# Kernel optimization log

Measured on AMD Instinct MI355X. Metric: run time of the kernel, lower is better.

## Reference

```python
import jax, jax.numpy as jnp
import numpy as np

N, C_IN, C_OUT, NS, SP = 100000, 64, 64, 16, 8
MID = C_OUT
EPS = 1e-5


def _bn(t, g, b):
    # BatchNorm1d training-mode stats over (n, k) per channel (biased var, as torch)
    m = t.mean(axis=(0, 1))
    v = t.var(axis=(0, 1))
    return g * (t - m) / jnp.sqrt(v + EPS) + b


def setup_inputs() -> dict:
    key = jax.random.key(0)
    ks = jax.random.split(key, 24)
    s = 0.05
    d = {
        'p': jax.random.normal(ks[0], (N, 3), jnp.float32),
        'x': jax.random.normal(ks[1], (N, C_IN), jnp.float32),
        'knn_idx': jax.random.randint(ks[2], (N, NS), 0, N, jnp.int64),
        # channelMixMLPs01: Linear(3+in, ns) + Bilinear(ns, ns, ns)
        'w1': jax.random.normal(ks[3], (NS, 3 + C_IN), jnp.float32) * s,
        'b1': jnp.zeros((NS,), jnp.float32),
        'bw': jax.random.normal(ks[4], (NS, NS, NS), jnp.float32) * s,
        'bb': jnp.zeros((NS,), jnp.float32),
        # linear_p: Linear(3,3) -> BN(3) -> ReLU -> Linear(3,out)
        'lp_w1': jax.random.normal(ks[5], (3, 3), jnp.float32) * s,
        'lp_b1': jnp.zeros((3,), jnp.float32),
        'bnp_g': jnp.ones((3,), jnp.float32),
        'bnp_b': jnp.zeros((3,), jnp.float32),
        'lp_w2': jax.random.normal(ks[6], (C_OUT, 3), jnp.float32) * s,
        'lp_b2': jnp.zeros((C_OUT,), jnp.float32),
        'c1_w': jax.random.normal(ks[7], (MID, 2 * NS), jnp.float32) * s,
        'bn1_g': jnp.ones((MID,), jnp.float32),
        'bn1_b': jnp.zeros((MID,), jnp.float32),
        'c2_w': jax.random.normal(ks[8], (MID // SP, MID), jnp.float32) * s,
        'bn2_g': jnp.ones((MID // SP,), jnp.float32),
        'bn2_b': jnp.zeros((MID // SP,), jnp.float32),
        'c3_w': jax.random.normal(ks[9], (C_OUT // SP, MID // SP), jnp.float32) * s,
        'c3_b': jnp.zeros((C_OUT // SP,), jnp.float32),
        # channelMixMLPs03: Linear(in, out)
        'w3': jax.random.normal(ks[10], (C_OUT, C_IN), jnp.float32) * s,
        'b3': jnp.zeros((C_OUT,), jnp.float32),
    }
    return d


def reference(p, x, knn_idx, w1, b1, bw, bb, lp_w1, lp_b1, bnp_g, bnp_b,
              lp_w2, lp_b2, c1_w, bn1_g, bn1_b, c2_w, bn2_g, bn2_b,
              c3_w, c3_b, w3, b3):
    n = p.shape[0]
    # queryandgroup (use_xyz=True): gather neighbors, relative coords + feats
    p_r = p[knn_idx] - p[:, None, :]                 # [n, k, 3]
    x_knn = jnp.concatenate([p_r, x[knn_idx]], -1)   # [n, k, 3+c_in]
    # channelMixMLPs01: Linear -> ReLU -> Bilinear(e, e)
    e = jax.nn.relu(x_knn @ w1.T + b1)               # [n, k, ns]
    e = jnp.einsum('nki,oij,nkj->nko', e, bw, e) + bb
    # linear_p on relative coords
    pe = p_r @ lp_w1.T + lp_b1                       # [n, k, 3]
    pe = jax.nn.relu(_bn(pe, bnp_g, bnp_b))
    p_embed = pe @ lp_w2.T + lp_b2                   # [n, k, out]
    # shrink_p: n k (a b) -> sum over a -> [n, k, ns]
    p_shrink = p_embed.reshape(n, NS, C_OUT // NS, NS).sum(axis=2)
    energy = jnp.concatenate([e, p_shrink], -1)
    # channelMixMLPs02 (1x1 convs == per-point linears over channel dim)
    h = jax.nn.relu(_bn(energy @ c1_w.T, bn1_g, bn1_b))
    h = jax.nn.relu(_bn(h @ c2_w.T, bn2_g, bn2_b))
    w = jax.nn.softmax(h @ c3_w.T + c3_b, axis=1)    # [n, k, out/sp]
    # value path: Linear then gather by knn_idx
    x_v = (x @ w3.T + b3)[knn_idx]                   # [n, k, out]
    xk = (x_v + p_embed).reshape(n, NS, SP, C_OUT // SP)
    xk = (xk * w[:, :, None, :]).reshape(n, NS, C_OUT)
    x_out = xk.sum(axis=1)                           # [n, out]
    return (x_out, xk, knn_idx, p_r)
```

## Files before the change

### kernel.cpp

```cpp
#include <hip/hip_runtime.h>
#include <math.h>

#define NPTS 100000
#define KNB  16
#define NK   1600000

#define OUT_XK   6400000
#define OUT_KNN  108800000
#define OUT_PR   110400000

#define WS_BNP_RAW 0
#define WS_BN2_RAW 134
#define WS_BNP_SS  160
#define WS_WS2     166
#define WS_WSB     214
#define WS_BN1_SS  230
#define WS_BN2_SS  358
#define WS_SYM     384
#define WS_C1F     2560
#define WS_C2T     2816
#define WS_GRAM    4096
#define WS_E       8192
#define WS_T2      25608192
#define WS_XROW    38408192
#define WS_X1      44808192

#define GRID_NK 3125
#define NK_STRIDE 800000

#define TA_PACK ((1ULL<<15)|(1ULL<<18)|(1ULL<<21)|(1ULL<<24)|(2ULL<<27)|(2ULL<<30)|(2ULL<<33)|(3ULL<<36)|(3ULL<<39)|(4ULL<<42))
#define TB_PACK ((1ULL<<3)|(2ULL<<6)|(3ULL<<9)|(4ULL<<12)|(1ULL<<15)|(2ULL<<18)|(3ULL<<21)|(4ULL<<24)|(2ULL<<27)|(3ULL<<30)|(4ULL<<33)|(3ULL<<36)|(4ULL<<39)|(4ULL<<42))


__global__ __launch_bounds__(256) void k_pre(
    const float* __restrict__ x, const float* __restrict__ w3,
    const float* __restrict__ b3, const float* __restrict__ w1,
    const float* __restrict__ b1, float* __restrict__ ws)
{
    int n = blockIdx.x * 256 + threadIdx.x;
    if (n >= NPTS) return;
    float xr[64];
    const float4* xp = (const float4*)(x + (size_t)n * 64);
    #pragma unroll
    for (int i = 0; i < 16; ++i) {
        float4 v = xp[i];
        xr[4*i] = v.x; xr[4*i+1] = v.y; xr[4*i+2] = v.z; xr[4*i+3] = v.w;
    }
    float* xrow = ws + WS_XROW;
    for (int c = 0; c < 64; ++c) {
        const float* wr = w3 + c * 64;
        float a0 = b3[c], a1 = 0.f;
        #pragma unroll
        for (int q = 0; q < 64; q += 2) { a0 += wr[q] * xr[q]; a1 += wr[q+1] * xr[q+1]; }
        xrow[(size_t)n * 64 + c] = a0 + a1;
    }
    float* X1 = ws + WS_X1;
    for (int j = 0; j < 16; ++j) {
        const float* wr = w1 + j * 67 + 3;
        float a0 = b1[j], a1 = 0.f;
        #pragma unroll
        for (int q = 0; q < 64; q += 2) { a0 += wr[q] * xr[q]; a1 += wr[q+1] * xr[q+1]; }
        X1[n * 16 + j] = a0 + a1;
    }
}

__global__ void k_sym(const float* __restrict__ bw, float* __restrict__ ws)
{
    int t = blockIdx.x * 256 + threadIdx.x;
    if (t >= 136 * 16) return;
    int pair = t >> 4, o = t & 15;
    int i = 0, r = pair;
    while (r >= 16 - i) { r -= 16 - i; ++i; }
    int j = i + r;
    float v = bw[o * 256 + i * 16 + j];
    if (i != j) v += bw[o * 256 + j * 16 + i];
    ws[WS_SYM + pair * 16 + o] = v;
}

__global__ __launch_bounds__(256) void k_pstats(
    const float* __restrict__ p, const int* __restrict__ knn,
    const float* __restrict__ lpw1, const float* __restrict__ lpb1,
    float* __restrict__ ws, float* __restrict__ out)
{
    float ps0=0.f, ps1=0.f, ps2=0.f, pq0=0.f, pq1=0.f, pq2=0.f;
    float* o_knn = out + OUT_KNN;
    float* o_pr  = out + OUT_PR;
    int id = blockIdx.x * 256 + threadIdx.x;
    #pragma unroll 1
    for (int it = 0; it < 2; ++it, id += NK_STRIDE) {
        int n = id >> 4;
        int idx = knn[id];
        float pr0 = p[idx*3+0] - p[n*3+0];
        float pr1 = p[idx*3+1] - p[n*3+1];
        float pr2 = p[idx*3+2] - p[n*3+2];
        o_pr[id*3+0] = pr0; o_pr[id*3+1] = pr1; o_pr[id*3+2] = pr2;
        o_knn[id] = (float)idx;
        float v0 = lpb1[0] + lpw1[0]*pr0 + lpw1[1]*pr1 + lpw1[2]*pr2;
        float v1 = lpb1[1] + lpw1[3]*pr0 + lpw1[4]*pr1 + lpw1[5]*pr2;
        float v2 = lpb1[2] + lpw1[6]*pr0 + lpw1[7]*pr1 + lpw1[8]*pr2;
        ps0 += v0; ps1 += v1; ps2 += v2;
        pq0 += v0*v0; pq1 += v1*v1; pq2 += v2*v2;
    }
    #pragma unroll
    for (int off = 32; off; off >>= 1) {
        ps0 += __shfl_xor(ps0, off); ps1 += __shfl_xor(ps1, off); ps2 += __shfl_xor(ps2, off);
        pq0 += __shfl_xor(pq0, off); pq1 += __shfl_xor(pq1, off); pq2 += __shfl_xor(pq2, off);
    }
    __shared__ float sb[6];
    if (threadIdx.x < 6) sb[threadIdx.x] = 0.f;
    __syncthreads();
    if ((threadIdx.x & 63) == 0) {
        atomicAdd(&sb[0], ps0); atomicAdd(&sb[1], ps1); atomicAdd(&sb[2], ps2);
        atomicAdd(&sb[3], pq0); atomicAdd(&sb[4], pq1); atomicAdd(&sb[5], pq2);
    }
    __syncthreads();
    if (threadIdx.x < 6) atomicAdd(&ws[WS_BNP_RAW + threadIdx.x], sb[threadIdx.x]);
}

__global__ void k_fin_bnp(float* __restrict__ ws,
    const float* __restrict__ g, const float* __restrict__ b,
    const float* __restrict__ lpw2, const float* __restrict__ lpb2)
{
    int t = threadIdx.x;
    if (t < 3) {
        float mean = ws[WS_BNP_RAW + t] / (float)NK;
        float var  = ws[WS_BNP_RAW + 3 + t] / (float)NK - mean * mean;
        float sc = g[t] * rsqrtf(var + 1e-5f);
        ws[WS_BNP_SS + t] = sc;
        ws[WS_BNP_SS + 3 + t] = b[t] - mean * sc;
    }
    if (t >= 16 && t < 64) {
        int r = t - 16, j = r / 3, d = r % 3;
        ws[WS_WS2 + r] = lpw2[(j)*3+d] + lpw2[(16+j)*3+d] + lpw2[(32+j)*3+d] + lpw2[(48+j)*3+d];
    }
    if (t >= 64 && t < 80) {
        int j = t - 64;
        ws[WS_WSB + j] = lpb2[j] + lpb2[16+j] + lpb2[32+j] + lpb2[48+j];
    }
}

__global__ void k_fold(const float* __restrict__ c1w, const float* __restrict__ c2w,
                       float* __restrict__ ws)
{
    int c = threadIdx.x;
    if (c >= 64) return;
    const float* B = c1w + c * 32 + 16;
    float m0 = 0.f, m1 = 0.f, m2 = 0.f, dd = 0.f;
    #pragma unroll
    for (int j = 0; j < 16; ++j) {
        float bj = B[j];
        m0 += bj * ws[WS_WS2 + j*3 + 0];
        m1 += bj * ws[WS_WS2 + j*3 + 1];
        m2 += bj * ws[WS_WS2 + j*3 + 2];
        dd += bj * ws[WS_WSB + j];
    }
    ws[WS_C1F + c*4 + 0] = m0;
    ws[WS_C1F + c*4 + 1] = m1;
    ws[WS_C1F + c*4 + 2] = m2;
    ws[WS_C1F + c*4 + 3] = dd;
    #pragma unroll
    for (int k = 0; k < 8; ++k)
        ws[WS_C2T + c*8 + k] = c2w[k * 64 + c];
}

__global__ __launch_bounds__(256) void k_stage0(
    const float* __restrict__ o_pr_in, const int* __restrict__ knn,
    const float* __restrict__ w1, const float* __restrict__ bb,
    const float* __restrict__ lpw1, const float* __restrict__ lpb1,
    const float* __restrict__ wsro, float* __restrict__ ws)
{
    __shared__ __align__(16) char uni[36864];
    float* e1sf  = (float*)uni;
    float* ub    = (float*)uni;
    float* gpart = (float*)(uni + 20480);
    const float* symw = wsro + WS_SYM;
    const float* X1   = wsro + WS_X1;
    float* e_out = ws + WS_E;
    int tid = threadIdx.x;

    int gid = blockIdx.x * 256 + tid;
    int id0 = gid * 2;
    float qv[2][3];

    #pragma unroll
    for (int e = 0; e < 2; ++e) {
        int id = id0 + e;
        int idx = knn[id];
        float pr0 = o_pr_in[id*3+0];
        float pr1 = o_pr_in[id*3+1];
        float pr2 = o_pr_in[id*3+2];
        float v0 = lpb1[0] + lpw1[0]*pr0 + lpw1[1]*pr1 + lpw1[2]*pr2;
        float v1 = lpb1[1] + lpw1[3]*pr0 + lpw1[4]*pr1 + lpw1[5]*pr2;
        float v2 = lpb1[2] + lpw1[6]*pr0 + lpw1[7]*pr1 + lpw1[8]*pr2;
        qv[e][0] = fmaxf(v0*wsro[WS_BNP_SS+0] + wsro[WS_BNP_SS+3], 0.f);
        qv[e][1] = fmaxf(v1*wsro[WS_BNP_SS+1] + wsro[WS_BNP_SS+4], 0.f);
        qv[e][2] = fmaxf(v2*wsro[WS_BNP_SS+2] + wsro[WS_BNP_SS+5], 0.f);
        const float4* xg = (const float4*)(X1 + (size_t)idx * 16);
        #pragma unroll
        for (int h = 0; h < 4; ++h) {
            float4 v = xg[h];
            const float* wr = w1 + (4*h) * 67;
            e1sf[e*4096 + (4*h+0)*256 + tid] = fmaxf(v.x + wr[0]*pr0 + wr[1]*pr1 + wr[2]*pr2, 0.f);
            wr += 67;
            e1sf[e*4096 + (4*h+1)*256 + tid] = fmaxf(v.y + wr[0]*pr0 + wr[1]*pr1 + wr[2]*pr2, 0.f);
            wr += 67;
            e1sf[e*4096 + (4*h+2)*256 + tid] = fmaxf(v.z + wr[0]*pr0 + wr[1]*pr1 + wr[2]*pr2, 0.f);
            wr += 67;
            e1sf[e*4096 + (4*h+3)*256 + tid] = fmaxf(v.w + wr[0]*pr0 + wr[1]*pr1 + wr[2]*pr2, 0.f);
        }
    }
    __syncthreads();

    float acc_a[16], acc_b[16];
    #pragma unroll
    for (int o = 0; o < 16; ++o) { float bo = bb[o]; acc_a[o] = bo; acc_b[o] = bo; }

    int pair = 0;
    #pragma unroll 1
    for (int i = 0; i < 16; ++i) {
        float eai = e1sf[i*256 + tid];
        float ebi = e1sf[4096 + i*256 + tid];
        #pragma unroll 2
        for (int j = i; j < 16; ++j, ++pair) {
            float eaj = e1sf[j*256 + tid];
            float ebj = e1sf[4096 + j*256 + tid];
            float ma = eai * eaj, mb = ebi * ebj;
            const float4* wp = (const float4*)(symw + pair * 16);
            float4 w0v = wp[0], w1v = wp[1], w2v = wp[2], w3v = wp[3];
            acc_a[0]  += w0v.x*ma; acc_a[1]  += w0v.y*ma; acc_a[2]  += w0v.z*ma; acc_a[3]  += w0v.w*ma;
            acc_a[4]  += w1v.x*ma; acc_a[5]  += w1v.y*ma; acc_a[6]  += w1v.z*ma; acc_a[7]  += w1v.w*ma;
            acc_a[8]  += w2v.x*ma; acc_a[9]  += w2v.y*ma; acc_a[10] += w2v.z*ma; acc_a[11] += w2v.w*ma;
            acc_a[12] += w3v.x*ma; acc_a[13] += w3v.y*ma; acc_a[14] += w3v.z*ma; acc_a[15] += w3v.w*ma;
            acc_b[0]  += w0v.x*mb; acc_b[1]  += w0v.y*mb; acc_b[2]  += w0v.z*mb; acc_b[3]  += w0v.w*mb;
            acc_b[4]  += w1v.x*mb; acc_b[5]  += w1v.y*mb; acc_b[6]  += w1v.z*mb; acc_b[7]  += w1v.w*mb;
            acc_b[8]  += w2v.x*mb; acc_b[9]  += w2v.y*mb; acc_b[10] += w2v.z*mb; acc_b[11] += w2v.w*mb;
            acc_b[12] += w3v.x*mb; acc_b[13] += w3v.y*mb; acc_b[14] += w3v.z*mb; acc_b[15] += w3v.w*mb;
        }
    }
    float4* eo = (float4*)(e_out + (size_t)id0 * 16);
    eo[0] = make_float4(acc_a[0],  acc_a[1],  acc_a[2],  acc_a[3]);
    eo[1] = make_float4(acc_a[4],  acc_a[5],  acc_a[6],  acc_a[7]);
    eo[2] = make_float4(acc_a[8],  acc_a[9],  acc_a[10], acc_a[11]);
    eo[3] = make_float4(acc_a[12], acc_a[13], acc_a[14], acc_a[15]);
    eo[4] = make_float4(acc_b[0],  acc_b[1],  acc_b[2],  acc_b[3]);
    eo[5] = make_float4(acc_b[4],  acc_b[5],  acc_b[6],  acc_b[7]);
    eo[6] = make_float4(acc_b[8],  acc_b[9],  acc_b[10], acc_b[11]);
    eo[7] = make_float4(acc_b[12], acc_b[13], acc_b[14], acc_b[15]);

    int l = tid & 15, g = tid >> 4;
    int tt = (l + g * 4) % 15;
    int a4 = (int)((TA_PACK >> (3*tt)) & 7) * 4;
    int b4 = (int)((TB_PACK >> (3*tt)) & 7) * 4;
    float gacc[16];
    #pragma unroll
    for (int k = 0; k < 16; ++k) gacc[k] = 0.f;

    #pragma unroll 1
    for (int rnd = 0; rnd < 2; ++rnd) {
        __syncthreads();
        if ((tid >> 7) == rnd) {
            int s0 = (tid & 127) * 2;
            #pragma unroll
            for (int e = 0; e < 2; ++e) {
                int s = s0 + e;
                const float* ac = e ? acc_b : acc_a;
                float u[20];
                #pragma unroll
                for (int k = 0; k < 16; ++k) u[k] = ac[k];
                u[16] = qv[e][0]; u[17] = qv[e][1]; u[18] = qv[e][2]; u[19] = 1.f;
                int rot = (s % 5) * 4;
                #pragma unroll
                for (int k = 0; k < 5; ++k) {
                    int phys = (4*k + rot) % 20;
                    *(float4*)(ub + s*20 + phys) = make_float4(u[4*k], u[4*k+1], u[4*k+2], u[4*k+3]);
                }
            }
        }
        __syncthreads();
        if (l < 15) {
            #pragma unroll 1
            for (int it2 = 0; it2 < 16; ++it2) {
                int s = g * 16 + it2;
                int rot = (s % 5) * 4;
                const float4 ua  = *(const float4*)(ub + s*20 + ((a4 + rot) % 20));
                const float4 ub4 = *(const float4*)(ub + s*20 + ((b4 + rot) % 20));
                gacc[0]  += ua.x*ub4.x; gacc[1]  += ua.x*ub4.y; gacc[2]  += ua.x*ub4.z; gacc[3]  += ua.x*ub4.w;
                gacc[4]  += ua.y*ub4.x; gacc[5]  += ua.y*ub4.y; gacc[6]  += ua.y*ub4.z; gacc[7]  += ua.y*ub4.w;
                gacc[8]  += ua.z*ub4.x; gacc[9]  += ua.z*ub4.y; gacc[10] += ua.z*ub4.z; gacc[11] += ua.z*ub4.w;
                gacc[12] += ua.w*ub4.x; gacc[13] += ua.w*ub4.y; gacc[14] += ua.w*ub4.z; gacc[15] += ua.w*ub4.w;
            }
        }
    }
    __syncthreads();
    if (l < 15) {
        #pragma unroll
        for (int k = 0; k < 16; ++k) gpart[tt*260 + k*16 + g] = gacc[k];
    }
    __syncthreads();
    if (tid < 240) {
        int t2 = tid >> 4, k2 = tid & 15;
        int base = t2 * 260 + k2 * 16;
        float s = 0.f;
        #pragma unroll
        for (int g2 = 0; g2 < 16; ++g2) s += gpart[base + g2];
        atomicAdd(&ws[WS_GRAM + (blockIdx.x & 7) * 240 + tid], s);
    }
}

__global__ __launch_bounds__(256) void k_fin_bn1(
    const float* __restrict__ c1w, const float* __restrict__ g,
    const float* __restrict__ b, float* __restrict__ ws)
{
    __shared__ float Gs[240];
    __shared__ float Gfull[400];
    __shared__ float Ach[64][21];
    int tid = threadIdx.x;
    if (tid < 240) {
        float s = 0.f;
        #pragma unroll
        for (int r = 0; r < 8; ++r) s += ws[WS_GRAM + r*240 + tid];
        Gs[tid] = s;
    }
    if (tid < 64) {
        #pragma unroll
        for (int k = 0; k < 16; ++k) Ach[tid][k] = c1w[tid*32 + k];
        Ach[tid][16] = ws[WS_C1F + tid*4 + 0];
        Ach[tid][17] = ws[WS_C1F + tid*4 + 1];
        Ach[tid][18] = ws[WS_C1F + tid*4 + 2];
        Ach[tid][19] = ws[WS_C1F + tid*4 + 3];
    }
    __syncthreads();
    for (int idx = tid; idx < 400; idx += 256) {
        int i = idx / 20, j = idx % 20;
        int a = i >> 2, ra = i & 3, bt = j >> 2, cb = j & 3;
        float v;
        if (a <= bt) {
            int t = a*5 - (a*(a-1))/2 + (bt - a);
            v = Gs[t*16 + ra*4 + cb];
        } else {
            int t = bt*5 - (bt*(bt-1))/2 + (a - bt);
            v = Gs[t*16 + cb*4 + ra];
        }
        Gfull[idx] = v;
    }
    __syncthreads();
    if (tid < 64) {
        float s1 = 0.f, ssq = 0.f;
        #pragma unroll 1
        for (int i = 0; i < 20; ++i) {
            float Ai = Ach[tid][i];
            s1 += Ai * Gfull[i*20 + 19];
            float inner = 0.f;
            #pragma unroll
            for (int j = 0; j < 20; ++j) inner += Ach[tid][j] * Gfull[i*20 + j];
            ssq += Ai * inner;
        }
        float mean = s1 / (float)NK;
        float var  = ssq / (float)NK - mean * mean;
        float sc = g[tid] * rsqrtf(var + 1e-5f);
        ws[WS_BN1_SS + tid] = sc;
        ws[WS_BN1_SS + 64 + tid] = b[tid] - mean * sc;
    }
}

__device__ __forceinline__ void build_eq(
    const float* __restrict__ e_in, const float* __restrict__ o_pr,
    const float* __restrict__ lpw1, const float* __restrict__ lpb1,
    const float* __restrict__ wsro, int id, float* e, float* q)
{
    const float4* ep = (const float4*)(e_in + (size_t)id * 16);
    #pragma unroll
    for (int i = 0; i < 4; ++i) {
        float4 v = ep[i];
        e[4*i] = v.x; e[4*i+1] = v.y; e[4*i+2] = v.z; e[4*i+3] = v.w;
    }
    float pr0 = o_pr[id*3+0], pr1 = o_pr[id*3+1], pr2 = o_pr[id*3+2];
    float v0 = lpb1[0] + lpw1[0]*pr0 + lpw1[1]*pr1 + lpw1[2]*pr2;
    float v1 = lpb1[1] + lpw1[3]*pr0 + lpw1[4]*pr1 + lpw1[5]*pr2;
    float v2 = lpb1[2] + lpw1[6]*pr0 + lpw1[7]*pr1 + lpw1[8]*pr2;
    q[0] = fmaxf(v0*wsro[WS_BNP_SS+0] + wsro[WS_BNP_SS+3], 0.f);
    q[1] = fmaxf(v1*wsro[WS_BNP_SS+1] + wsro[WS_BNP_SS+4], 0.f);
    q[2] = fmaxf(v2*wsro[WS_BNP_SS+2] + wsro[WS_BNP_SS+5], 0.f);
}

__global__ __launch_bounds__(256) void k_stage2(
    const float* __restrict__ wsro, const float* __restrict__ out_ro,
    const float* __restrict__ lpw1, const float* __restrict__ lpb1,
    const float* __restrict__ c1w, float* __restrict__ ws)
{
    float tsum[8] = {0,0,0,0,0,0,0,0}, tssq[8] = {0,0,0,0,0,0,0,0};
    const float* e_in = wsro + WS_E;
    const float* o_pr = out_ro + OUT_PR;
    float* t2 = ws + WS_T2;
    int id = blockIdx.x * 256 + threadIdx.x;
    #pragma unroll 1
    for (int it = 0; it < 2; ++it, id += NK_STRIDE) {
        float e[16], q[3];
        build_eq(e_in, o_pr, lpw1, lpb1, wsro, id, e, q);
        float t2a[8] = {0,0,0,0,0,0,0,0};
        #pragma unroll 1
        for (int c = 0; c < 64; c += 2) {
            const float* wa = c1w + c * 32;
            const float* wb = wa + 32;
            const float4 fa = *(const float4*)(wsro + WS_C1F + c*4);
            const float4 fb = *(const float4*)(wsro + WS_C1F + c*4 + 4);
            float h0 = fa.w + fa.x*q[0] + fa.y*q[1] + fa.z*q[2];
            float h1 = fb.w + fb.x*q[0] + fb.y*q[1] + fb.z*q[2];
            #pragma unroll
            for (int k = 0; k < 16; ++k) {
                h0 += wa[k]*e[k]; h1 += wb[k]*e[k];
            }
            h0 = fmaxf(h0 * wsro[WS_BN1_SS + c]     + wsro[WS_BN1_SS + 64 + c], 0.f);
            h1 = fmaxf(h1 * wsro[WS_BN1_SS + c + 1] + wsro[WS_BN1_SS + 65 + c], 0.f);
            const float4 ca0 = *(const float4*)(wsro + WS_C2T + c*8);
            const float4 ca1 = *(const float4*)(wsro + WS_C2T + c*8 + 4);
            const float4 cb0 = *(const float4*)(wsro + WS_C2T + c*8 + 8);
            const float4 cb1 = *(const float4*)(wsro + WS_C2T + c*8 + 12);
            t2a[0] += h0*ca0.x + h1*cb0.x; t2a[1] += h0*ca0.y + h1*cb0.y;
            t2a[2] += h0*ca0.z + h1*cb0.z; t2a[3] += h0*ca0.w + h1*cb0.w;
            t2a[4] += h0*ca1.x + h1*cb1.x; t2a[5] += h0*ca1.y + h1*cb1.y;
            t2a[6] += h0*ca1.z + h1*cb1.z; t2a[7] += h0*ca1.w + h1*cb1.w;
        }
        float4* t2p = (float4*)(t2 + (size_t)id * 8);
        t2p[0] = make_float4(t2a[0], t2a[1], t2a[2], t2a[3]);
        t2p[1] = make_float4(t2a[4], t2a[5], t2a[6], t2a[7]);
        #pragma unroll
        for (int c2 = 0; c2 < 8; ++c2) { tsum[c2] += t2a[c2]; tssq[c2] += t2a[c2] * t2a[c2]; }
    }
    __shared__ float sacc[16];
    if (threadIdx.x < 16) sacc[threadIdx.x] = 0.f;
    __syncthreads();
    #pragma unroll
    for (int c2 = 0; c2 < 8; ++c2) {
        float s = tsum[c2], s2 = tssq[c2];
        #pragma unroll
        for (int off = 32; off; off >>= 1) { s += __shfl_xor(s, off); s2 += __shfl_xor(s2, off); }
        if ((threadIdx.x & 63) == 0) { atomicAdd(&sacc[c2], s); atomicAdd(&sacc[8 + c2], s2); }
    }
    __syncthreads();
    if (threadIdx.x < 16) atomicAdd(&ws[WS_BN2_RAW + threadIdx.x], sacc[threadIdx.x]);
}

__global__ void k_fin_bn2(float* __restrict__ ws, const float* __restrict__ g, const float* __restrict__ b)
{
    int c = threadIdx.x;
    if (c < 8) {
        float mean = ws[WS_BN2_RAW + c] / (float)NK;
        float var  = ws[WS_BN2_RAW + 8 + c] / (float)NK - mean * mean;
        float sc = g[c] * rsqrtf(var + 1e-5f);
        ws[WS_BN2_SS + c] = sc;
        ws[WS_BN2_SS + 8 + c] = b[c] - mean * sc;
    }
}

__global__ __launch_bounds__(256) void k_final(
    const int* __restrict__ knn, const float* __restrict__ wsro,
    const float* __restrict__ c3w, const float* __restrict__ c3b,
    const float* __restrict__ lpw1, const float* __restrict__ lpb1,
    const float* __restrict__ lpw2, const float* __restrict__ lpb2,
    float* __restrict__ out)
{
    int t = threadIdx.x;
    int sub = t >> 7, tl = t & 127;
    int n = blockIdx.x * 2 + sub;
    __shared__ float h2s[2][16][8], ssm[2][16][8], wls[2][16][8], pes[2][16][3], prs[2][48], red[2][128];
    __shared__ int idxs[2][16];
    const float* t2   = wsro + WS_T2;
    const float* o_pr = out + OUT_PR;
    const float* xrow = wsro + WS_XROW;
    if (tl < 16) idxs[sub][tl] = knn[n * 16 + tl];
    if (tl < 48) prs[sub][tl] = o_pr[(size_t)n * 48 + tl];
    {
        int k = tl >> 3, c2 = tl & 7;
        float v = t2[(size_t)n * 128 + tl];
        h2s[sub][k][c2] = fmaxf(v * wsro[WS_BN2_SS + c2] + wsro[WS_BN2_SS + 8 + c2], 0.f);
    }
    __syncthreads();
    if (tl < 48) {
        int k = tl / 3, d = tl % 3;
        float pe = lpb1[d] + lpw1[d*3+0]*prs[sub][k*3+0] + lpw1[d*3+1]*prs[sub][k*3+1] + lpw1[d*3+2]*prs[sub][k*3+2];
        pes[sub][k][d] = fmaxf(pe * wsro[WS_BNP_SS + d] + wsro[WS_BNP_SS + 3 + d], 0.f);
    }
    {
        int k = tl >> 3, cc = tl & 7;
        float s = c3b[cc];
        #pragma unroll
        for (int q = 0; q < 8; ++q) s += h2s[sub][k][q] * c3w[cc * 8 + q];
        ssm[sub][k][cc] = s;
    }
    __syncthreads();
    if (tl < 8) {
        float m = -1e30f;
        for (int k = 0; k < 16; ++k) m = fmaxf(m, ssm[sub][k][tl]);
        float sum = 0.f;
        for (int k = 0; k < 16; ++k) { float ev = __expf(ssm[sub][k][tl] - m); wls[sub][k][tl] = ev; sum += ev; }
        float inv = 1.f / sum;
        for (int k = 0; k < 16; ++k) wls[sub][k][tl] *= inv;
    }
    __syncthreads();
    int c = tl & 63, kh = tl >> 6;
    float w20 = lpw2[c*3], w21 = lpw2[c*3+1], w22 = lpw2[c*3+2], bc = lpb2[c];
    float acc = 0.f;
    float* out_xk = out + OUT_XK + (size_t)n * 1024;
    #pragma unroll
    for (int i = 0; i < 8; ++i) {
        int k = kh * 8 + i;
        float xv = xrow[(size_t)idxs[sub][k] * 64 + c];
        float pemb = bc + w20 * pes[sub][k][0] + w21 * pes[sub][k][1] + w22 * pes[sub][k][2];
        float val = (xv + pemb) * wls[sub][k][c & 7];
        out_xk[k * 64 + c] = val;
        acc += val;
    }
    red[sub][tl] = acc;
    __syncthreads();
    if (tl < 64) out[(size_t)n * 64 + tl] = red[sub][tl] + red[sub][tl + 64];
}

extern "C" void kernel_launch(void* const* d_in, const int* in_sizes, int n_in,
                              void* d_out, int out_size, void* d_ws, size_t ws_size,
                              hipStream_t stream)
{
    (void)in_sizes; (void)n_in; (void)out_size; (void)ws_size;
    const float* p    = (const float*)d_in[0];
    const float* x    = (const float*)d_in[1];
    const int*   knn  = (const int*)  d_in[2];
    const float* w1   = (const float*)d_in[3];
    const float* b1   = (const float*)d_in[4];
    const float* bw   = (const float*)d_in[5];
    const float* bb   = (const float*)d_in[6];
    const float* lpw1 = (const float*)d_in[7];
    const float* lpb1 = (const float*)d_in[8];
    const float* bnpg = (const float*)d_in[9];
    const float* bnpb = (const float*)d_in[10];
    const float* lpw2 = (const float*)d_in[11];
    const float* lpb2 = (const float*)d_in[12];
    const float* c1w  = (const float*)d_in[13];
    const float* bn1g = (const float*)d_in[14];
    const float* bn1b = (const float*)d_in[15];
    const float* c2w  = (const float*)d_in[16];
    const float* bn2g = (const float*)d_in[17];
    const float* bn2b = (const float*)d_in[18];
    const float* c3w  = (const float*)d_in[19];
    const float* c3b  = (const float*)d_in[20];
    const float* w3   = (const float*)d_in[21];
    const float* b3   = (const float*)d_in[22];
    float* out = (float*)d_out;
    float* ws  = (float*)d_ws;

    (void)hipMemsetAsync(ws, 0, 6016 * sizeof(float), stream);
    k_pre   <<<(NPTS + 255) / 256, 256, 0, stream>>>(x, w3, b3, w1, b1, ws);
    k_sym   <<<9, 256, 0, stream>>>(bw, ws);
    k_pstats<<<GRID_NK, 256, 0, stream>>>(p, knn, lpw1, lpb1, ws, out);
    k_fin_bnp<<<1, 128, 0, stream>>>(ws, bnpg, bnpb, lpw2, lpb2);
    k_fold  <<<1, 64, 0, stream>>>(c1w, c2w, ws);
    k_stage0<<<GRID_NK, 256, 0, stream>>>(out + OUT_PR, knn, w1, bb, lpw1, lpb1, ws, ws);
    k_fin_bn1<<<1, 256, 0, stream>>>(c1w, bn1g, bn1b, ws);
    k_stage2<<<GRID_NK, 256, 0, stream>>>(ws, out, lpw1, lpb1, c1w, ws);
    k_fin_bn2<<<1, 64, 0, stream>>>(ws, bn2g, bn2b);
    k_final <<<NPTS / 2, 256, 0, stream>>>(knn, ws, c3w, c3b, lpw1, lpb1, lpw2, lpb2, out);
}
```

Before: 587.3 us.

## Pack four points per block in final kernel and restructure stage2 conv loop

k_final now assigns one 64-thread wavefront per point and four points per block, so each thread walks all 16 neighbours and writes the summed output directly, with no shared-memory reduction. Each thread also handles two neighbour rows in the h2 and softmax-logit setup. In k_stage2 the c1 loop processes four output channels per iteration and splits each dot product into two accumulators to shorten the FMA dependency chains. The aim is fewer blocks, less synchronisation and more ILP, at the cost of a longer serial gather loop per thread and higher register use in stage2.

```diff
diff --git a/kernel.cpp b/kernel.cpp
--- a/kernel.cpp
+++ b/kernel.cpp
@@ -399,27 +399,31 @@
         build_eq(e_in, o_pr, lpw1, lpb1, wsro, id, e, q);
         float t2a[8] = {0,0,0,0,0,0,0,0};
         #pragma unroll 1
-        for (int c = 0; c < 64; c += 2) {
-            const float* wa = c1w + c * 32;
-            const float* wb = wa + 32;
-            const float4 fa = *(const float4*)(wsro + WS_C1F + c*4);
-            const float4 fb = *(const float4*)(wsro + WS_C1F + c*4 + 4);
-            float h0 = fa.w + fa.x*q[0] + fa.y*q[1] + fa.z*q[2];
-            float h1 = fb.w + fb.x*q[0] + fb.y*q[1] + fb.z*q[2];
+        for (int c = 0; c < 64; c += 4) {
+            float h[4];
             #pragma unroll
-            for (int k = 0; k < 16; ++k) {
-                h0 += wa[k]*e[k]; h1 += wb[k]*e[k];
+            for (int r = 0; r < 4; ++r) {
+                const float* wr = c1w + (c + r) * 32;
+                const float4 fr = *(const float4*)(wsro + WS_C1F + (c + r) * 4);
+                float a0 = fr.w + fr.x*q[0] + fr.y*q[1] + fr.z*q[2];
+                float a1 = 0.f;
+                #pragma unroll
+                for (int k = 0; k < 16; k += 2) {
+                    a0 += wr[k] * e[k];
+                    a1 += wr[k+1] * e[k+1];
+                }
+                h[r] = fmaxf((a0 + a1) * wsro[WS_BN1_SS + c + r] + wsro[WS_BN1_SS + 64 + c + r], 0.f);
             }
-            h0 = fmaxf(h0 * wsro[WS_BN1_SS + c]     + wsro[WS_BN1_SS + 64 + c], 0.f);
-            h1 = fmaxf(h1 * wsro[WS_BN1_SS + c + 1] + wsro[WS_BN1_SS + 65 + c], 0.f);
-            const float4 ca0 = *(const float4*)(wsro + WS_C2T + c*8);
-            const float4 ca1 = *(const float4*)(wsro + WS_C2T + c*8 + 4);
-            const float4 cb0 = *(const float4*)(wsro + WS_C2T + c*8 + 8);
-            const float4 cb1 = *(const float4*)(wsro + WS_C2T + c*8 + 12);
-            t2a[0] += h0*ca0.x + h1*cb0.x; t2a[1] += h0*ca0.y + h1*cb0.y;
-            t2a[2] += h0*ca0.z + h1*cb0.z; t2a[3] += h0*ca0.w + h1*cb0.w;
-            t2a[4] += h0*ca1.x + h1*cb1.x; t2a[5] += h0*ca1.y + h1*cb1.y;
-            t2a[6] += h0*ca1.z + h1*cb1.z; t2a[7] += h0*ca1.w + h1*cb1.w;
+            #pragma unroll
+            for (int r = 0; r < 4; ++r) {
+                const float4 cr0 = *(const float4*)(wsro + WS_C2T + (c + r) * 8);
+                const float4 cr1 = *(const float4*)(wsro + WS_C2T + (c + r) * 8 + 4);
+                float hh = h[r];
+                t2a[0] += hh * cr0.x; t2a[1] += hh * cr0.y;
+                t2a[2] += hh * cr0.z; t2a[3] += hh * cr0.w;
+                t2a[4] += hh * cr1.x; t2a[5] += hh * cr1.y;
+                t2a[6] += hh * cr1.z; t2a[7] += hh * cr1.w;
+            }
         }
         float4* t2p = (float4*)(t2 + (size_t)id * 8);
         t2p[0] = make_float4(t2a[0], t2a[1], t2a[2], t2a[3]);
@@ -461,10 +465,10 @@
     float* __restrict__ out)
 {
     int t = threadIdx.x;
-    int sub = t >> 7, tl = t & 127;
-    int n = blockIdx.x * 2 + sub;
-    __shared__ float h2s[2][16][8], ssm[2][16][8], wls[2][16][8], pes[2][16][3], prs[2][48], red[2][128];
-    __shared__ int idxs[2][16];
+    int sub = t >> 6, tl = t & 63;
+    int n = blockIdx.x * 4 + sub;
+    __shared__ float h2s[4][16][8], ssm[4][16][8], wls[4][16][8], pes[4][16][3], prs[4][48];
+    __shared__ int idxs[4][16];
     const float* t2   = wsro + WS_T2;
     const float* o_pr = out + OUT_PR;
     const float* xrow = wsro + WS_XROW;
@@ -472,8 +476,10 @@
     if (tl < 48) prs[sub][tl] = o_pr[(size_t)n * 48 + tl];
     {
         int k = tl >> 3, c2 = tl & 7;
-        float v = t2[(size_t)n * 128 + tl];
-        h2s[sub][k][c2] = fmaxf(v * wsro[WS_BN2_SS + c2] + wsro[WS_BN2_SS + 8 + c2], 0.f);
+        float v0 = t2[(size_t)n * 128 + tl];
+        float v1 = t2[(size_t)n * 128 + 64 + tl];
+        h2s[sub][k][c2]     = fmaxf(v0 * wsro[WS_BN2_SS + c2] + wsro[WS_BN2_SS + 8 + c2], 0.f);
+        h2s[sub][8 + k][c2] = fmaxf(v1 * wsro[WS_BN2_SS + c2] + wsro[WS_BN2_SS + 8 + c2], 0.f);
     }
     __syncthreads();
     if (tl < 48) {
@@ -483,10 +489,14 @@
     }
     {
         int k = tl >> 3, cc = tl & 7;
-        float s = c3b[cc];
-        #pragma unroll
-        for (int q = 0; q < 8; ++q) s += h2s[sub][k][q] * c3w[cc * 8 + q];
-        ssm[sub][k][cc] = s;
+        float s0 = c3b[cc], s1 = c3b[cc];
+        #pragma unroll
+        for (int q = 0; q < 8; ++q) {
+            s0 += h2s[sub][k][q]     * c3w[cc * 8 + q];
+            s1 += h2s[sub][8 + k][q] * c3w[cc * 8 + q];
+        }
+        ssm[sub][k][cc] = s0;
+        ssm[sub][8 + k][cc] = s1;
     }
     __syncthreads();
     if (tl < 8) {
@@ -498,22 +508,19 @@
         for (int k = 0; k < 16; ++k) wls[sub][k][tl] *= inv;
     }
     __syncthreads();
-    int c = tl & 63, kh = tl >> 6;
+    int c = tl;
     float w20 = lpw2[c*3], w21 = lpw2[c*3+1], w22 = lpw2[c*3+2], bc = lpb2[c];
     float acc = 0.f;
     float* out_xk = out + OUT_XK + (size_t)n * 1024;
-    #pragma unroll
-    for (int i = 0; i < 8; ++i) {
-        int k = kh * 8 + i;
+    #pragma unroll 1
+    for (int k = 0; k < 16; ++k) {
         float xv = xrow[(size_t)idxs[sub][k] * 64 + c];
         float pemb = bc + w20 * pes[sub][k][0] + w21 * pes[sub][k][1] + w22 * pes[sub][k][2];
         float val = (xv + pemb) * wls[sub][k][c & 7];
         out_xk[k * 64 + c] = val;
         acc += val;
     }
-    red[sub][tl] = acc;
-    __syncthreads();
-    if (tl < 64) out[(size_t)n * 64 + tl] = red[sub][tl] + red[sub][tl + 64];
+    out[(size_t)n * 64 + c] = acc;
 }
 
 extern "C" void kernel_launch(void* const* d_in, const int* in_sizes, int n_in,
@@ -557,5 +564,5 @@
     k_fin_bn1<<<1, 256, 0, stream>>>(c1w, bn1g, bn1b, ws);
     k_stage2<<<GRID_NK, 256, 0, stream>>>(ws, out, lpw1, lpb1, c1w, ws);
     k_fin_bn2<<<1, 64, 0, stream>>>(ws, bn2g, bn2b);
-    k_final <<<NPTS / 2, 256, 0, stream>>>(knn, ws, c3w, c3b, lpw1, lpb1, lpw2, lpb2, out);
-}
+    k_final <<<NPTS / 4, 256, 0, stream>>>(knn, ws, c3w, c3b, lpw1, lpb1, lpw2, lpb2, out);
+}
```

New measurement: 583.7 us. No clear change (-0.6%).
